# Kernel tuning notes

Measured on AMD Instinct MI355X. Metric: run time of the kernel, lower is better.

## Reference

```python
import jax, jax.numpy as jnp
import numpy as np

N = 3  # lateral kernel size (hardcoded in original call via i:i+3 slices)


def _center_zero_mask(n, dtype):
    # ones everywhere except the center tap (the layer excludes self-connection)
    m = jnp.ones((n, n), dtype=dtype)
    return m.at[n // 2, n // 2].set(0.0)


def setup_inputs() -> dict:
    key = jax.random.key(0)
    kx, kk = jax.random.split(key)
    B, H, W, C = 32, 56, 56, 256
    x = jax.random.normal(kx, (B, H, W, C), dtype=jnp.float32)
    # glorot-ish scale for a (3,3,C) depthwise kernel
    kernel = jax.random.normal(kk, (N, N, C), dtype=jnp.float32) * 0.1
    return {"x": x, "kernel": kernel}


def reference(x, kernel):
    # x: [B,H,W,C], kernel: [n,n,C] (one n x n filter per channel)
    n, _, ch = kernel.shape
    masked = kernel * _center_zero_mask(n, kernel.dtype)[:, :, None]  # zero center tap
    # depthwise conv: HWIO with I=1, feature_group_count=C
    w = masked.reshape(n, n, 1, ch)
    out = jax.lax.conv_general_dilated(
        x, w,
        window_strides=(1, 1),
        padding="SAME",
        dimension_numbers=("NHWC", "HWIO", "NHWC"),
        feature_group_count=ch,
    )
    return out + x  # residual add
```

## Files before the change

kernel.cpp:

```cpp
#include <hip/hip_runtime.h>


#define BB 32
#define HH 56
#define WW 56
#define CC 256
#define C4 (CC / 4)
#define NXCD 8
#define P 14
#define NHC (HH / P)
#define ROWSTR (WW * C4)

#define FMA4(acc, v, k)          \
    acc.x += (v).x * (k).x;      \
    acc.y += (v).y * (k).y;      \
    acc.z += (v).z * (k).z;      \
    acc.w += (v).w * (k).w;

__global__ __launch_bounds__(256, 4) void contour_kernel(
    const float4* __restrict__ x,
    const float4* __restrict__ kern,
    float4* __restrict__ out)
{
    const int nblocks = gridDim.x;
    const int per_xcd = nblocks / NXCD;
    const int xcd     = blockIdx.x % NXCD;
    const int local   = blockIdx.x / NXCD;
    const int blk     = xcd * per_xcd + local;

    int idx = blk * blockDim.x + threadIdx.x;
    int c4 = idx & (C4 - 1);
    int s  = idx >> 6;
    int w  = s % WW;
    int t  = s / WW;
    int hc = t & (NHC - 1);
    int b  = t >> 2;
    if (b >= BB) return;

    const float4 zero = make_float4(0.f, 0.f, 0.f, 0.f);

    const float4* kp = kern + c4;
    float4 k0 = kp[0 * C4], k1 = kp[1 * C4], k2 = kp[2 * C4];
    float4 k3 = kp[3 * C4],                  k5 = kp[5 * C4];
    float4 k6 = kp[6 * C4], k7 = kp[7 * C4], k8 = kp[8 * C4];

    const int h0 = hc * P;
    const float4* xb = x   + (size_t)(b * HH) * ROWSTR + w * C4 + c4;
    float4*       ob = out + (size_t)(b * HH) * ROWSTR + w * C4 + c4;

    const bool wl = (w > 0);
    const bool wr = (w < WW - 1);

    float4 a0, a1, a2, r0, r1, r2, c0, c1, c2;

    auto loadrow = [&](int hh, float4& L, float4& Cv, float4& R) {
        if (hh < 0 || hh >= HH) { L = zero; Cv = zero; R = zero; return; }
        const float4* p = xb + hh * ROWSTR;
        Cv = p[0];
        L  = wl ? p[-C4] : zero;
        R  = wr ? p[ C4] : zero;
    };

    loadrow(h0 - 1, a0, a1, a2);
    loadrow(h0,     r0, r1, r2);

    #pragma unroll
    for (int i = 0; i < P; ++i) {
        const int h = h0 + i;
        loadrow(h + 1, c0, c1, c2);

        float4 acc = r1;
        FMA4(acc, a0, k0); FMA4(acc, a1, k1); FMA4(acc, a2, k2);
        FMA4(acc, r0, k3);                    FMA4(acc, r2, k5);
        FMA4(acc, c0, k6); FMA4(acc, c1, k7); FMA4(acc, c2, k8);

        ob[h * ROWSTR] = acc;

        a0 = r0; a1 = r1; a2 = r2;
        r0 = c0; r1 = c1; r2 = c2;
    }
}

extern "C" void kernel_launch(void* const* d_in, const int* in_sizes, int n_in,
                              void* d_out, int out_size, void* d_ws, size_t ws_size,
                              hipStream_t stream) {
    const float4* x    = (const float4*)d_in[0];
    const float4* kern = (const float4*)d_in[1];
    float4* out        = (float4*)d_out;

    const int total = BB * NHC * WW * C4;
    const int block = 256;
    const int grid  = (total + block - 1) / block;
    contour_kernel<<<grid, block, 0, stream>>>(x, kern, out);
}
```

Before: 194.6 us.

## Restructure depthwise stencil into scatter-style partial sums to cut register pressure

Replaces the rolling three-row window (nine float4 registers) with two running partial-sum accumulators. Each input row is loaded once and added into the outputs it contributes to, as the top, middle or bottom row of their stencil. This cuts live registers, and the launch bounds are raised to ask for more waves per SIMD, aiming for more memory-level parallelism on this bandwidth-bound kernel. Empty asm statements pin the kernel taps in registers. The out-of-range batch guard is removed, which relies on the grid dividing evenly.

```diff
diff --git a/kernel.cpp b/kernel.cpp
--- a/kernel.cpp
+++ b/kernel.cpp
@@ -4,20 +4,41 @@
 #define BB 32
 #define HH 56
 #define WW 56
-#define CC 256
-#define C4 (CC / 4)
+#define C4 64
 #define NXCD 8
 #define P 14
-#define NHC (HH / P)
+#define NHC 4
 #define ROWSTR (WW * C4)
 
-#define FMA4(acc, v, k)          \
-    acc.x += (v).x * (k).x;      \
-    acc.y += (v).y * (k).y;      \
-    acc.z += (v).z * (k).z;      \
-    acc.w += (v).w * (k).w;
+#define KEEP4(v) asm volatile("" : "+v"((v).x), "+v"((v).y), "+v"((v).z), "+v"((v).w))
 
-__global__ __launch_bounds__(256, 4) void contour_kernel(
+#define CALC_T(d)                                   \
+    (d).x = k0.x*Lv.x + k1.x*Cv.x + k2.x*Rv.x;      \
+    (d).y = k0.y*Lv.y + k1.y*Cv.y + k2.y*Rv.y;      \
+    (d).z = k0.z*Lv.z + k1.z*Cv.z + k2.z*Rv.z;      \
+    (d).w = k0.w*Lv.w + k1.w*Cv.w + k2.w*Rv.w;
+
+#define ADD_M(d)                                    \
+    (d).x += Cv.x + k3.x*Lv.x + k5.x*Rv.x;          \
+    (d).y += Cv.y + k3.y*Lv.y + k5.y*Rv.y;          \
+    (d).z += Cv.z + k3.z*Lv.z + k5.z*Rv.z;          \
+    (d).w += Cv.w + k3.w*Lv.w + k5.w*Rv.w;
+
+#define ADD_B(d)                                    \
+    (d).x += k6.x*Lv.x + k7.x*Cv.x + k8.x*Rv.x;     \
+    (d).y += k6.y*Lv.y + k7.y*Cv.y + k8.y*Rv.y;     \
+    (d).z += k6.z*Lv.z + k7.z*Cv.z + k8.z*Rv.z;     \
+    (d).w += k6.w*Lv.w + k7.w*Cv.w + k8.w*Rv.w;
+
+#define LOADROW(y)                                  \
+    {                                               \
+        const float4* p = xb + (y) * ROWSTR;        \
+        Cv = p[0];                                  \
+        Lv = wl ? p[-C4] : zero;                    \
+        Rv = wr ? p[ C4] : zero;                    \
+    }
+
+__global__ __launch_bounds__(256, 7) void contour_kernel(
     const float4* __restrict__ x,
     const float4* __restrict__ kern,
     float4* __restrict__ out)
@@ -35,7 +56,6 @@
     int t  = s / WW;
     int hc = t & (NHC - 1);
     int b  = t >> 2;
-    if (b >= BB) return;
 
     const float4 zero = make_float4(0.f, 0.f, 0.f, 0.f);
 
@@ -43,6 +63,8 @@
     float4 k0 = kp[0 * C4], k1 = kp[1 * C4], k2 = kp[2 * C4];
     float4 k3 = kp[3 * C4],                  k5 = kp[5 * C4];
     float4 k6 = kp[6 * C4], k7 = kp[7 * C4], k8 = kp[8 * C4];
+    KEEP4(k0); KEEP4(k1); KEEP4(k2); KEEP4(k3);
+    KEEP4(k5); KEEP4(k6); KEEP4(k7); KEEP4(k8);
 
     const int h0 = hc * P;
     const float4* xb = x   + (size_t)(b * HH) * ROWSTR + w * C4 + c4;
@@ -51,34 +73,38 @@
     const bool wl = (w > 0);
     const bool wr = (w < WW - 1);
 
-    float4 a0, a1, a2, r0, r1, r2, c0, c1, c2;
+    float4 Lv, Cv, Rv;
+    float4 pA;
+    float4 pB;
 
-    auto loadrow = [&](int hh, float4& L, float4& Cv, float4& R) {
-        if (hh < 0 || hh >= HH) { L = zero; Cv = zero; R = zero; return; }
-        const float4* p = xb + hh * ROWSTR;
-        Cv = p[0];
-        L  = wl ? p[-C4] : zero;
-        R  = wr ? p[ C4] : zero;
-    };
+    if (h0 > 0) {
+        LOADROW(h0 - 1);
+        CALC_T(pB);
+    } else {
+        pB = zero;
+    }
 
-    loadrow(h0 - 1, a0, a1, a2);
-    loadrow(h0,     r0, r1, r2);
+    LOADROW(h0);
+    ADD_M(pB);
+    pA = pB;
+    CALC_T(pB);
 
     #pragma unroll
-    for (int i = 0; i < P; ++i) {
-        const int h = h0 + i;
-        loadrow(h + 1, c0, c1, c2);
+    for (int j = 1; j <= P - 1; ++j) {
+        const int y = h0 + j;
+        LOADROW(y);
+        ADD_B(pA);
+        ob[(y - 1) * ROWSTR] = pA;
+        ADD_M(pB);
+        pA = pB;
+        CALC_T(pB);
+    }
 
-        float4 acc = r1;
-        FMA4(acc, a0, k0); FMA4(acc, a1, k1); FMA4(acc, a2, k2);
-        FMA4(acc, r0, k3);                    FMA4(acc, r2, k5);
-        FMA4(acc, c0, k6); FMA4(acc, c1, k7); FMA4(acc, c2, k8);
-
-        ob[h * ROWSTR] = acc;
-
-        a0 = r0; a1 = r1; a2 = r2;
-        r0 = c0; r1 = c1; r2 = c2;
+    if (h0 + P < HH) {
+        LOADROW(h0 + P);
+        ADD_B(pA);
     }
+    ob[(h0 + P - 1) * ROWSTR] = pA;
 }
 
 extern "C" void kernel_launch(void* const* d_in, const int* in_sizes, int n_in,
```

Result: slower. 280.3 us (+44.0%).
